# Performance work log

Hardware: AMD Instinct MI355X
Metric: run time of the kernel (lower is better)

Reference implementation:

```python
import jax, jax.numpy as jnp
import numpy as np

B, CW_DIM, Z_DIM = 512, 4096, 1024
DIM_CODES, BOOK_SIZE, DIM_EMBED = 64, 1024, 64
ENC_H, DEC_H = 512, 2048
SLOPE = 0.2  # LeakyReLU negative slope

def lrelu(v):
    return jnp.where(v > 0, v, SLOPE * v)

def setup_inputs() -> dict:
    key = jax.random.key(0)
    ks = jax.random.split(key, 12)
    s = 0.02
    inp = {
        'x': jax.random.normal(ks[0], (B, CW_DIM), jnp.float32),
        'codebook': jax.random.normal(ks[1], (DIM_CODES, BOOK_SIZE, DIM_EMBED), jnp.float32),
        'enc_w1': jax.random.normal(ks[2], (ENC_H, DIM_EMBED), jnp.float32) * s,
        'enc_b1': jnp.zeros((ENC_H,), jnp.float32),
        'enc_w2': jax.random.normal(ks[3], (2 * Z_DIM, ENC_H), jnp.float32) * s,
        'enc_b2': jnp.zeros((2 * Z_DIM,), jnp.float32),
        'inf1_w': jax.random.normal(ks[4], (Z_DIM // 2, 2 * Z_DIM), jnp.float32) * s,
        'inf1_b': jnp.zeros((Z_DIM // 2,), jnp.float32),
        'inf2_w1': jax.random.normal(ks[5], (2 * Z_DIM, 9 * Z_DIM // 4), jnp.float32) * s,
        'inf2_b1': jnp.zeros((2 * Z_DIM,), jnp.float32),
        'inf2_w2': jax.random.normal(ks[6], (3 * Z_DIM // 2, 2 * Z_DIM), jnp.float32) * s,
        'inf2_b2': jnp.zeros((3 * Z_DIM // 2,), jnp.float32),
        'prior_w1': jax.random.normal(ks[7], (2 * Z_DIM, Z_DIM // 4), jnp.float32) * s,
        'prior_b1': jnp.zeros((2 * Z_DIM,), jnp.float32),
        'prior_w2': jax.random.normal(ks[8], (3 * Z_DIM // 2, 2 * Z_DIM), jnp.float32) * s,
        'prior_b2': jnp.zeros((3 * Z_DIM // 2,), jnp.float32),
        'dec_w1': jax.random.normal(ks[9], (DEC_H, 3 * Z_DIM // 4), jnp.float32) * s,
        'dec_b1': jnp.zeros((DEC_H,), jnp.float32),
        'dec_w2': jax.random.normal(ks[10], (CW_DIM, DEC_H), jnp.float32) * s,
        'dec_b2': jnp.zeros((CW_DIM,), jnp.float32),
    }
    return inp

def reference(x, codebook, enc_w1, enc_b1, enc_w2, enc_b2,
              inf1_w, inf1_b, inf2_w1, inf2_b1, inf2_w2, inf2_b2,
              prior_w1, prior_b1, prior_w2, prior_b2,
              dec_w1, dec_b1, dec_w2, dec_b2):
    b = x.shape[0]
    # ---- encode: view (B, dim_codes, dim_embed), per-code conv + max-pool + Linear
    xe = x.reshape(b, DIM_CODES, DIM_EMBED)                       # (B, C, E)
    feat = lrelu(jnp.einsum('bce,he->bch', xe, enc_w1) + enc_b1)  # (B, C, H)
    h = jnp.max(feat, axis=1) @ enc_w2.T + enc_b2                 # (B, 2z)
    mu, log_var = jnp.split(h @ inf1_w.T + inf1_b, 2, axis=1)     # (B, z/4) each
    z1 = mu                                                        # eval mode: sample == mu
    # ---- decode
    p = lrelu(z1 @ prior_w1.T + prior_b1) @ prior_w2.T + prior_b2
    p_mu, p_logvar = jnp.split(p, 2, axis=1)                       # (B, 3z/4) each
    d = lrelu(jnp.concatenate([z1, h], axis=1) @ inf2_w1.T + inf2_b1) @ inf2_w2.T + inf2_b2
    d_mu, d_log_var = jnp.split(d, 2, axis=1)
    z2 = d_mu + p_mu                                               # eval mode sample
    cw_recon = lrelu(z2 @ dec_w1.T + dec_b1) @ dec_w2.T + dec_b2   # (B, cw_dim)
    # ---- dist: squared distance to (detached) codebook, no explicit repeat
    xr = cw_recon.reshape(b, DIM_CODES, DIM_EMBED)
    book = jax.lax.stop_gradient(codebook)                         # (C, S, E)
    cw_dist = ((xr ** 2).sum(-1)[..., None]
               + (book ** 2).sum(-1)[None]
               - 2.0 * jnp.einsum('bce,cse->bcs', xr, book))       # (B, C, S)
    idx = jnp.argmin(cw_dist, axis=-1).reshape(b * DIM_CODES, 1)   # matches torch (B*C, 1)
    return (cw_recon, cw_dist, idx, mu, log_var, d_mu, d_log_var, p_logvar)
```

## Files before the change

kernel.cpp:

```cpp
#include <hip/hip_runtime.h>
#include <hip/hip_bf16.h>

typedef __hip_bfloat16 bf16;
typedef unsigned short u16;

#define BATCH 512
#define CW_DIM 4096
#define DIM_CODES 64
#define BOOK_SIZE 1024
#define DIM_EMBED 64
#define ENC_H 512

__device__ __forceinline__ float bf2f(u16 u) {
    unsigned int x = ((unsigned int)u) << 16;
    return __uint_as_float(x);
}
__device__ __forceinline__ float loadf(const void* p, size_t i, int bf) {
    if (bf) return bf2f(((const u16*)p)[i]);
    return ((const float*)p)[i];
}
__device__ __forceinline__ float4 load4(const void* p, size_t i, int bf) {
    if (bf) {
        const u16* q = (const u16*)p + i;
        uint2 raw = *reinterpret_cast<const uint2*>(q);
        float4 r;
        r.x = bf2f((u16)(raw.x & 0xFFFF));
        r.y = bf2f((u16)(raw.x >> 16));
        r.z = bf2f((u16)(raw.y & 0xFFFF));
        r.w = bf2f((u16)(raw.y >> 16));
        return r;
    }
    return *reinterpret_cast<const float4*>((const float*)p + i);
}
__device__ __forceinline__ void stored(void* p, size_t i, int bf, double v) {
    if (bf) ((bf16*)p)[i] = __float2bfloat16((float)v);
    else    ((float*)p)[i] = (float)v;
}
__device__ __forceinline__ u16 f2bfu(float v) {
    bf16 b = __float2bfloat16(v);
    return *reinterpret_cast<u16*>(&b);
}

__global__ void detect_kernel(const u16* __restrict__ x, int* __restrict__ flag) {
    __shared__ int hits;
    if (threadIdx.x == 0) hits = 0;
    __syncthreads();
    int h = 0;
    for (int i = threadIdx.x; i < 16384; i += 256) {
        u16 v = x[2 * i];
        if (((v >> 7) & 0xFF) == 0xFF) h++;
    }
    atomicAdd(&hits, h);
    __syncthreads();
    if (threadIdx.x == 0) *flag = (hits == 0) ? 1 : 0;
}

__global__ void booknorm_kernel(const void* __restrict__ book, double* __restrict__ bn,
                                const int* __restrict__ dflag) {
    const int bf = *dflag;
    int r = blockIdx.x * blockDim.x + threadIdx.x;
    if (r >= DIM_CODES * BOOK_SIZE) return;
    double acc = 0.0;
    for (int e = 0; e < DIM_EMBED; e += 4) {
        float4 v = load4(book, (size_t)r * DIM_EMBED + e, bf);
        acc = fma((double)v.x, (double)v.x, acc);
        acc = fma((double)v.y, (double)v.y, acc);
        acc = fma((double)v.z, (double)v.z, acc);
        acc = fma((double)v.w, (double)v.w, acc);
    }
    bn[r] = acc;
}

__global__ __launch_bounds__(256) void enc_kernel(const void* __restrict__ x,
                                                  const void* __restrict__ w1,
                                                  const void* __restrict__ b1,
                                                  float* __restrict__ hmax,
                                                  const int* __restrict__ dflag) {
    const int bf = *dflag;
    __shared__ float xs_t[64][68];
    __shared__ float wsh_t[64][68];
    __shared__ float red[64][17];
    int t = threadIdx.x;
    int h0 = blockIdx.x * 64;
    int b = blockIdx.y;

    int cr = t >> 2;
    int e0 = (t & 3) << 4;
    for (int q = 0; q < 4; q++) {
        int e = e0 + (q << 2);
        float4 xv = load4(x, (size_t)b * CW_DIM + cr * DIM_EMBED + e, bf);
        xs_t[e + 0][cr] = xv.x; xs_t[e + 1][cr] = xv.y;
        xs_t[e + 2][cr] = xv.z; xs_t[e + 3][cr] = xv.w;
        float4 wv = load4(w1, (size_t)(h0 + cr) * DIM_EMBED + e, bf);
        wsh_t[e + 0][cr] = wv.x; wsh_t[e + 1][cr] = wv.y;
        wsh_t[e + 2][cr] = wv.z; wsh_t[e + 3][cr] = wv.w;
    }
    __syncthreads();

    int th = t & 15, tc = t >> 4;
    float acc[4][4] = {};
    for (int e = 0; e < 64; e++) {
        float4 a4 = *(const float4*)&xs_t[e][tc << 2];
        float4 w4 = *(const float4*)&wsh_t[e][th << 2];
        float aa[4] = {a4.x, a4.y, a4.z, a4.w};
        float ww[4] = {w4.x, w4.y, w4.z, w4.w};
#pragma unroll
        for (int i = 0; i < 4; i++)
#pragma unroll
            for (int j = 0; j < 4; j++)
                acc[i][j] = fmaf(aa[i], ww[j], acc[i][j]);
    }
#pragma unroll
    for (int j = 0; j < 4; j++) {
        float bj = loadf(b1, h0 + (th << 2) + j, bf);
        float m = -1e30f;
#pragma unroll
        for (int i = 0; i < 4; i++) {
            float v = acc[i][j] + bj;
            v = v > 0.f ? v : 0.2f * v;
            m = fmaxf(m, v);
        }
        red[(th << 2) + j][tc] = m;
    }
    __syncthreads();
    if (t < 64) {
        float m = red[t][0];
        for (int k = 1; k < 16; k++) m = fmaxf(m, red[t][k]);
        hmax[(size_t)b * ENC_H + h0 + t] = m;
    }
}

__global__ __launch_bounds__(256) void gemm_kernel(const float* __restrict__ A1, int lda1, int K1,
                                                   const float* __restrict__ A2, int lda2, int Ktot,
                                                   const float* __restrict__ Aadd,
                                                   const void* __restrict__ W,
                                                   const void* __restrict__ bias,
                                                   float* __restrict__ C, int N, int act,
                                                   void* __restrict__ out,
                                                   size_t s0base, int s0c0, int s0c1, int s0stride,
                                                   size_t s1base, int s1c0, int s1c1, int s1stride,
                                                   const int* __restrict__ dflag) {
    const int bf = *dflag;
    __shared__ float As[2][16][68];
    __shared__ float Ws[2][16][68];
    int t = threadIdx.x;
    int tx = t & 15, ty = t >> 4;
    int n0 = blockIdx.x * 64, m0 = blockIdx.y * 64;
    int mrow = t >> 2, kq = (t & 3) << 2;
    float acc[4][4] = {};

    float4 av, wv;
    {
        int k = kq;
        if (k < K1) {
            av = *reinterpret_cast<const float4*>(A1 + (size_t)(m0 + mrow) * lda1 + k);
            if (Aadd) {
                float4 ad = *reinterpret_cast<const float4*>(Aadd + (size_t)(m0 + mrow) * lda1 + k);
                av.x += ad.x; av.y += ad.y; av.z += ad.z; av.w += ad.w;
            }
        } else {
            av = *reinterpret_cast<const float4*>(A2 + (size_t)(m0 + mrow) * lda2 + (k - K1));
        }
        wv = load4(W, (size_t)(n0 + mrow) * Ktot + k, bf);
    }
    As[0][kq + 0][mrow] = av.x; As[0][kq + 1][mrow] = av.y;
    As[0][kq + 2][mrow] = av.z; As[0][kq + 3][mrow] = av.w;
    Ws[0][kq + 0][mrow] = wv.x; Ws[0][kq + 1][mrow] = wv.y;
    Ws[0][kq + 2][mrow] = wv.z; Ws[0][kq + 3][mrow] = wv.w;
    __syncthreads();

    int buf = 0;
#pragma unroll 1
    for (int kt = 0; kt < Ktot; kt += 16) {
        int nxt = kt + 16;
        if (nxt < Ktot) {
            int k = nxt + kq;
            if (k < K1) {
                av = *reinterpret_cast<const float4*>(A1 + (size_t)(m0 + mrow) * lda1 + k);
                if (Aadd) {
                    float4 ad = *reinterpret_cast<const float4*>(Aadd + (size_t)(m0 + mrow) * lda1 + k);
                    av.x += ad.x; av.y += ad.y; av.z += ad.z; av.w += ad.w;
                }
            } else {
                av = *reinterpret_cast<const float4*>(A2 + (size_t)(m0 + mrow) * lda2 + (k - K1));
            }
            wv = load4(W, (size_t)(n0 + mrow) * Ktot + k, bf);
        }
#pragma unroll
        for (int kk = 0; kk < 16; kk++) {
            float4 a4 = *(const float4*)&As[buf][kk][ty << 2];
            float4 w4 = *(const float4*)&Ws[buf][kk][tx << 2];
            float a[4] = {a4.x, a4.y, a4.z, a4.w};
            float w[4] = {w4.x, w4.y, w4.z, w4.w};
#pragma unroll
            for (int i = 0; i < 4; i++)
#pragma unroll
                for (int j = 0; j < 4; j++)
                    acc[i][j] = fmaf(a[i], w[j], acc[i][j]);
        }
        if (nxt < Ktot) {
            int nb = buf ^ 1;
            As[nb][kq + 0][mrow] = av.x; As[nb][kq + 1][mrow] = av.y;
            As[nb][kq + 2][mrow] = av.z; As[nb][kq + 3][mrow] = av.w;
            Ws[nb][kq + 0][mrow] = wv.x; Ws[nb][kq + 1][mrow] = wv.y;
            Ws[nb][kq + 2][mrow] = wv.z; Ws[nb][kq + 3][mrow] = wv.w;
            __syncthreads();
            buf = nb;
        }
    }

    int nbase = n0 + tx * 4;
    float b0 = loadf(bias, nbase + 0, bf), b1v = loadf(bias, nbase + 1, bf);
    float b2 = loadf(bias, nbase + 2, bf), b3 = loadf(bias, nbase + 3, bf);
#pragma unroll
    for (int i = 0; i < 4; i++) {
        int m = m0 + ty * 4 + i;
        float ov[4];
        ov[0] = acc[i][0] + b0; ov[1] = acc[i][1] + b1v;
        ov[2] = acc[i][2] + b2; ov[3] = acc[i][3] + b3;
        if (act) {
#pragma unroll
            for (int j = 0; j < 4; j++) ov[j] = ov[j] > 0.f ? ov[j] : 0.2f * ov[j];
        }
        float4 o = {ov[0], ov[1], ov[2], ov[3]};
        *reinterpret_cast<float4*>(C + (size_t)m * N + nbase) = o;
        if (nbase >= s0c0 && nbase < s0c1) {
            size_t off = s0base + (size_t)m * s0stride + (nbase - s0c0);
            if (bf) {
                ushort4 h = {f2bfu(ov[0]), f2bfu(ov[1]), f2bfu(ov[2]), f2bfu(ov[3])};
                *reinterpret_cast<ushort4*>((u16*)out + off) = h;
            } else {
                *reinterpret_cast<float4*>((float*)out + off) = o;
            }
        }
        if (nbase >= s1c0 && nbase < s1c1) {
            size_t off = s1base + (size_t)m * s1stride + (nbase - s1c0);
            if (bf) {
                ushort4 h = {f2bfu(ov[0]), f2bfu(ov[1]), f2bfu(ov[2]), f2bfu(ov[3])};
                *reinterpret_cast<ushort4*>((u16*)out + off) = h;
            } else {
                *reinterpret_cast<float4*>((float*)out + off) = o;
            }
        }
    }
}

__global__ __launch_bounds__(256, 4) void dist_kernel(const float* __restrict__ cwr,
                                                      const void* __restrict__ book,
                                                      const double* __restrict__ bn,
                                                      void* __restrict__ out,
                                                      size_t odist, size_t oidx,
                                                      const int* __restrict__ dflag) {
    const int bf = *dflag;
    __shared__ double xs[32][64];
    __shared__ double xn[32];
    __shared__ float bs[64][66];
    int t = threadIdx.x;
    int c = blockIdx.x;
    int b0 = blockIdx.y * 32;
    int sl = t & 63, wv = t >> 6;

    for (int i = t; i < 32 * 64; i += 256) {
        int bl = i >> 6, e = i & 63;
        xs[bl][e] = (double)cwr[(size_t)(b0 + bl) * CW_DIM + c * DIM_EMBED + e];
    }
    __syncthreads();
    if (t < 32) {
        double a = 0.0;
        for (int e = 0; e < 64; e++) a = fma(xs[t][e], xs[t][e], a);
        xn[t] = a;
    }

    double bd[8];
    int bsx[8];
#pragma unroll
    for (int p = 0; p < 8; p++) { bd[p] = 1e300; bsx[p] = 0; }

#pragma unroll 1
    for (int st = 0; st < 16; st++) {
        int s0 = st * 64;
        __syncthreads();
#pragma unroll
        for (int i4 = t; i4 < 1024; i4 += 256) {
            int srow = i4 >> 4, e4 = (i4 & 15) << 2;
            float4 v = load4(book, ((size_t)c * BOOK_SIZE + s0 + srow) * DIM_EMBED + e4, bf);
            bs[srow][e4 + 0] = v.x; bs[srow][e4 + 1] = v.y;
            bs[srow][e4 + 2] = v.z; bs[srow][e4 + 3] = v.w;
        }
        __syncthreads();
        double bnv = bn[(size_t)c * BOOK_SIZE + s0 + sl];
#pragma unroll
        for (int pb = 0; pb < 2; pb++) {
            int blb = wv * 8 + pb * 4;
            double a0 = 0.0, a1 = 0.0, a2 = 0.0, a3 = 0.0;
#pragma unroll 8
            for (int e = 0; e < 64; e += 2) {
                float2 bv = *(const float2*)&bs[sl][e];
                double bv0 = (double)bv.x, bv1 = (double)bv.y;
                double2 x0 = *(const double2*)&xs[blb + 0][e];
                double2 x1 = *(const double2*)&xs[blb + 1][e];
                double2 x2 = *(const double2*)&xs[blb + 2][e];
                double2 x3 = *(const double2*)&xs[blb + 3][e];
                a0 = fma(x0.x, bv0, a0); a0 = fma(x0.y, bv1, a0);
                a1 = fma(x1.x, bv0, a1); a1 = fma(x1.y, bv1, a1);
                a2 = fma(x2.x, bv0, a2); a2 = fma(x2.y, bv1, a2);
                a3 = fma(x3.x, bv0, a3); a3 = fma(x3.y, bv1, a3);
            }
            double dv[4];
            dv[0] = a0; dv[1] = a1; dv[2] = a2; dv[3] = a3;
#pragma unroll
            for (int j = 0; j < 4; j++) {
                int bl = blb + j;
                double d = xn[bl] + bnv - 2.0 * dv[j];
                stored(out, odist + ((size_t)(b0 + bl) * DIM_CODES + c) * BOOK_SIZE + s0 + sl, bf, d);
                if (d < bd[pb * 4 + j]) { bd[pb * 4 + j] = d; bsx[pb * 4 + j] = s0 + sl; }
            }
        }
    }
#pragma unroll
    for (int p = 0; p < 8; p++) {
        double d = bd[p];
        int s = bsx[p];
        for (int off = 32; off >= 1; off >>= 1) {
            double od = __shfl_xor(d, off, 64);
            int os = __shfl_xor(s, off, 64);
            if (od < d || (od == d && os < s)) { d = od; s = os; }
        }
        if (sl == 0)
            stored(out, oidx + (size_t)(b0 + wv * 8 + p) * DIM_CODES + c, bf, (double)s);
    }
}

extern "C" void kernel_launch(void* const* d_in, const int* in_sizes, int n_in,
                              void* d_out, int out_size, void* d_ws, size_t ws_size,
                              hipStream_t stream) {
    const void* x        = d_in[0];
    const void* codebook = d_in[1];
    const void* enc_w1   = d_in[2];
    const void* enc_b1   = d_in[3];
    const void* enc_w2   = d_in[4];
    const void* enc_b2   = d_in[5];
    const void* inf1_w   = d_in[6];
    const void* inf1_b   = d_in[7];
    const void* inf2_w1  = d_in[8];
    const void* inf2_b1  = d_in[9];
    const void* inf2_w2  = d_in[10];
    const void* inf2_b2  = d_in[11];
    const void* prior_w1 = d_in[12];
    const void* prior_b1 = d_in[13];
    const void* prior_w2 = d_in[14];
    const void* prior_b2 = d_in[15];
    const void* dec_w1   = d_in[16];
    const void* dec_b1   = d_in[17];
    const void* dec_w2   = d_in[18];
    const void* dec_b2   = d_in[19];

    float* W0 = (float*)d_ws;
    float* inf1out = W0;
    float* pfull   = inf1out + 262144;
    float* dfull   = pfull + 786432;
    float* cwr     = dfull + 786432;
    float* bufA    = cwr + 2097152;
    float* bufB    = bufA + 1048576;
    float* bufC    = bufB + 1048576;
    double* bn     = (double*)(bufC + 393216);
    int* dflag     = (int*)(bn + 65536);

    const size_t o_cwrecon = 0;
    const size_t o_cwdist  = 2097152;
    const size_t o_idx     = 35651584;
    const size_t o_mu      = 35684352;
    const size_t o_logvar  = 35815424;
    const size_t o_dmu     = 35946496;
    const size_t o_dlogvar = 36339712;
    const size_t o_plogvar = 36732928;

    detect_kernel<<<1, 256, 0, stream>>>((const u16*)x, dflag);
    booknorm_kernel<<<256, 256, 0, stream>>>(codebook, bn, dflag);
    enc_kernel<<<dim3(8, BATCH), 256, 0, stream>>>(x, enc_w1, enc_b1, bufC, dflag);

    gemm_kernel<<<dim3(32, 8), 256, 0, stream>>>(bufC, 512, 512, bufC, 512, 512, nullptr,
                                                 enc_w2, enc_b2, bufA, 2048, 0,
                                                 d_out, 0, 0, 0, 0, 0, 0, 0, 0, dflag);
    gemm_kernel<<<dim3(8, 8), 256, 0, stream>>>(bufA, 2048, 2048, bufA, 2048, 2048, nullptr,
                                                inf1_w, inf1_b, inf1out, 512, 0,
                                                d_out, o_mu, 0, 256, 256,
                                                o_logvar, 256, 512, 256, dflag);
    gemm_kernel<<<dim3(32, 8), 256, 0, stream>>>(inf1out, 512, 256, inf1out, 512, 256, nullptr,
                                                 prior_w1, prior_b1, bufB, 2048, 1,
                                                 d_out, 0, 0, 0, 0, 0, 0, 0, 0, dflag);
    gemm_kernel<<<dim3(24, 8), 256, 0, stream>>>(bufB, 2048, 2048, bufB, 2048, 2048, nullptr,
                                                 prior_w2, prior_b2, pfull, 1536, 0,
                                                 d_out, o_plogvar, 768, 1536, 768,
                                                 0, 0, 0, 0, dflag);
    gemm_kernel<<<dim3(32, 8), 256, 0, stream>>>(inf1out, 512, 256, bufA, 2048, 2304, nullptr,
                                                 inf2_w1, inf2_b1, bufB, 2048, 1,
                                                 d_out, 0, 0, 0, 0, 0, 0, 0, 0, dflag);
    gemm_kernel<<<dim3(24, 8), 256, 0, stream>>>(bufB, 2048, 2048, bufB, 2048, 2048, nullptr,
                                                 inf2_w2, inf2_b2, dfull, 1536, 0,
                                                 d_out, o_dmu, 0, 768, 768,
                                                 o_dlogvar, 768, 1536, 768, dflag);
    gemm_kernel<<<dim3(32, 8), 256, 0, stream>>>(dfull, 1536, 768, dfull, 1536, 768, pfull,
                                                 dec_w1, dec_b1, bufA, 2048, 1,
                                                 d_out, 0, 0, 0, 0, 0, 0, 0, 0, dflag);
    gemm_kernel<<<dim3(64, 8), 256, 0, stream>>>(bufA, 2048, 2048, bufA, 2048, 2048, nullptr,
                                                 dec_w2, dec_b2, cwr, 4096, 0,
                                                 d_out, o_cwrecon, 0, 4096, 4096,
                                                 0, 0, 0, 0, dflag);

    dist_kernel<<<dim3(64, 16), 256, 0, stream>>>(cwr, codebook, bn,
                                                  d_out, o_cwdist, o_idx, dflag);
}
```

Baseline: 1.068 ms.

## Batch independent prior/inference GEMMs into paired launches and double-buffer codebook tiles

Independent GEMM pairs (prior and inf2 layers) now run together in one launch through a descriptor-based gemm2 kernel, with a new scratch buffer so both outputs can coexist. This removes two launches and fills the GPU better, since each single GEMM alone had a small grid. The distance kernel now double-buffers codebook tiles in shared memory, prefetching the next tile into registers while computing the current one, to hide global load latency. The cost is more LDS per block, which may lower occupancy in the dist kernel, and more registers for the prefetch.

```diff
diff --git a/kernel.cpp b/kernel.cpp
--- a/kernel.cpp
+++ b/kernel.cpp
@@ -130,38 +130,37 @@
     }
 }
 
-__global__ __launch_bounds__(256) void gemm_kernel(const float* __restrict__ A1, int lda1, int K1,
-                                                   const float* __restrict__ A2, int lda2, int Ktot,
-                                                   const float* __restrict__ Aadd,
-                                                   const void* __restrict__ W,
-                                                   const void* __restrict__ bias,
-                                                   float* __restrict__ C, int N, int act,
-                                                   void* __restrict__ out,
-                                                   size_t s0base, int s0c0, int s0c1, int s0stride,
-                                                   size_t s1base, int s1c0, int s1c1, int s1stride,
-                                                   const int* __restrict__ dflag) {
-    const int bf = *dflag;
+struct GDesc {
+    const float* A1; const float* A2; const float* Aadd;
+    const void* W; const void* bias; float* C;
+    int lda1, K1, lda2, Ktot, N, act, nbx, pad;
+    size_t s0base; int s0c0, s0c1, s0stride;
+    size_t s1base; int s1c0, s1c1, s1stride;
+};
+
+__device__ __forceinline__ void gemm_body(const GDesc& g, int bx, int by,
+                                          void* __restrict__ out, const int bf) {
     __shared__ float As[2][16][68];
     __shared__ float Ws[2][16][68];
     int t = threadIdx.x;
     int tx = t & 15, ty = t >> 4;
-    int n0 = blockIdx.x * 64, m0 = blockIdx.y * 64;
+    int n0 = bx * 64, m0 = by * 64;
     int mrow = t >> 2, kq = (t & 3) << 2;
     float acc[4][4] = {};
 
     float4 av, wv;
     {
         int k = kq;
-        if (k < K1) {
-            av = *reinterpret_cast<const float4*>(A1 + (size_t)(m0 + mrow) * lda1 + k);
-            if (Aadd) {
-                float4 ad = *reinterpret_cast<const float4*>(Aadd + (size_t)(m0 + mrow) * lda1 + k);
+        if (k < g.K1) {
+            av = *reinterpret_cast<const float4*>(g.A1 + (size_t)(m0 + mrow) * g.lda1 + k);
+            if (g.Aadd) {
+                float4 ad = *reinterpret_cast<const float4*>(g.Aadd + (size_t)(m0 + mrow) * g.lda1 + k);
                 av.x += ad.x; av.y += ad.y; av.z += ad.z; av.w += ad.w;
             }
         } else {
-            av = *reinterpret_cast<const float4*>(A2 + (size_t)(m0 + mrow) * lda2 + (k - K1));
-        }
-        wv = load4(W, (size_t)(n0 + mrow) * Ktot + k, bf);
+            av = *reinterpret_cast<const float4*>(g.A2 + (size_t)(m0 + mrow) * g.lda2 + (k - g.K1));
+        }
+        wv = load4(g.W, (size_t)(n0 + mrow) * g.Ktot + k, bf);
     }
     As[0][kq + 0][mrow] = av.x; As[0][kq + 1][mrow] = av.y;
     As[0][kq + 2][mrow] = av.z; As[0][kq + 3][mrow] = av.w;
@@ -171,20 +170,20 @@
 
     int buf = 0;
 #pragma unroll 1
-    for (int kt = 0; kt < Ktot; kt += 16) {
+    for (int kt = 0; kt < g.Ktot; kt += 16) {
         int nxt = kt + 16;
-        if (nxt < Ktot) {
+        if (nxt < g.Ktot) {
             int k = nxt + kq;
-            if (k < K1) {
-                av = *reinterpret_cast<const float4*>(A1 + (size_t)(m0 + mrow) * lda1 + k);
-                if (Aadd) {
-                    float4 ad = *reinterpret_cast<const float4*>(Aadd + (size_t)(m0 + mrow) * lda1 + k);
+            if (k < g.K1) {
+                av = *reinterpret_cast<const float4*>(g.A1 + (size_t)(m0 + mrow) * g.lda1 + k);
+                if (g.Aadd) {
+                    float4 ad = *reinterpret_cast<const float4*>(g.Aadd + (size_t)(m0 + mrow) * g.lda1 + k);
                     av.x += ad.x; av.y += ad.y; av.z += ad.z; av.w += ad.w;
                 }
             } else {
-                av = *reinterpret_cast<const float4*>(A2 + (size_t)(m0 + mrow) * lda2 + (k - K1));
-            }
-            wv = load4(W, (size_t)(n0 + mrow) * Ktot + k, bf);
+                av = *reinterpret_cast<const float4*>(g.A2 + (size_t)(m0 + mrow) * g.lda2 + (k - g.K1));
+            }
+            wv = load4(g.W, (size_t)(n0 + mrow) * g.Ktot + k, bf);
         }
 #pragma unroll
         for (int kk = 0; kk < 16; kk++) {
@@ -198,7 +197,7 @@
                 for (int j = 0; j < 4; j++)
                     acc[i][j] = fmaf(a[i], w[j], acc[i][j]);
         }
-        if (nxt < Ktot) {
+        if (nxt < g.Ktot) {
             int nb = buf ^ 1;
             As[nb][kq + 0][mrow] = av.x; As[nb][kq + 1][mrow] = av.y;
             As[nb][kq + 2][mrow] = av.z; As[nb][kq + 3][mrow] = av.w;
@@ -210,22 +209,22 @@
     }
 
     int nbase = n0 + tx * 4;
-    float b0 = loadf(bias, nbase + 0, bf), b1v = loadf(bias, nbase + 1, bf);
-    float b2 = loadf(bias, nbase + 2, bf), b3 = loadf(bias, nbase + 3, bf);
+    float b0 = loadf(g.bias, nbase + 0, bf), b1v = loadf(g.bias, nbase + 1, bf);
+    float b2 = loadf(g.bias, nbase + 2, bf), b3 = loadf(g.bias, nbase + 3, bf);
 #pragma unroll
     for (int i = 0; i < 4; i++) {
         int m = m0 + ty * 4 + i;
         float ov[4];
         ov[0] = acc[i][0] + b0; ov[1] = acc[i][1] + b1v;
         ov[2] = acc[i][2] + b2; ov[3] = acc[i][3] + b3;
-        if (act) {
+        if (g.act) {
 #pragma unroll
             for (int j = 0; j < 4; j++) ov[j] = ov[j] > 0.f ? ov[j] : 0.2f * ov[j];
         }
         float4 o = {ov[0], ov[1], ov[2], ov[3]};
-        *reinterpret_cast<float4*>(C + (size_t)m * N + nbase) = o;
-        if (nbase >= s0c0 && nbase < s0c1) {
-            size_t off = s0base + (size_t)m * s0stride + (nbase - s0c0);
+        *reinterpret_cast<float4*>(g.C + (size_t)m * g.N + nbase) = o;
+        if (nbase >= g.s0c0 && nbase < g.s0c1) {
+            size_t off = g.s0base + (size_t)m * g.s0stride + (nbase - g.s0c0);
             if (bf) {
                 ushort4 h = {f2bfu(ov[0]), f2bfu(ov[1]), f2bfu(ov[2]), f2bfu(ov[3])};
                 *reinterpret_cast<ushort4*>((u16*)out + off) = h;
@@ -233,8 +232,8 @@
                 *reinterpret_cast<float4*>((float*)out + off) = o;
             }
         }
-        if (nbase >= s1c0 && nbase < s1c1) {
-            size_t off = s1base + (size_t)m * s1stride + (nbase - s1c0);
+        if (nbase >= g.s1c0 && nbase < g.s1c1) {
+            size_t off = g.s1base + (size_t)m * g.s1stride + (nbase - g.s1c0);
             if (bf) {
                 ushort4 h = {f2bfu(ov[0]), f2bfu(ov[1]), f2bfu(ov[2]), f2bfu(ov[3])};
                 *reinterpret_cast<ushort4*>((u16*)out + off) = h;
@@ -243,6 +242,20 @@
             }
         }
     }
+}
+
+__global__ __launch_bounds__(256) void gemm_kernel(GDesc g, void* __restrict__ out,
+                                                   const int* __restrict__ dflag) {
+    gemm_body(g, blockIdx.x, blockIdx.y, out, *dflag);
+}
+
+__global__ __launch_bounds__(256) void gemm2_kernel(GDesc g0, GDesc g1, void* __restrict__ out,
+                                                    const int* __restrict__ dflag) {
+    const int bf = *dflag;
+    bool first = (int)blockIdx.x < g0.nbx;
+    GDesc g = first ? g0 : g1;
+    int bx = first ? blockIdx.x : blockIdx.x - g0.nbx;
+    gemm_body(g, bx, blockIdx.y, out, bf);
 }
 
 __global__ __launch_bounds__(256, 4) void dist_kernel(const float* __restrict__ cwr,
@@ -254,7 +267,7 @@
     const int bf = *dflag;
     __shared__ double xs[32][64];
     __shared__ double xn[32];
-    __shared__ float bs[64][66];
+    __shared__ float bs[2][64][66];
     int t = threadIdx.x;
     int c = blockIdx.x;
     int b0 = blockIdx.y * 32;
@@ -264,12 +277,33 @@
         int bl = i >> 6, e = i & 63;
         xs[bl][e] = (double)cwr[(size_t)(b0 + bl) * CW_DIM + c * DIM_EMBED + e];
     }
+    {
+        size_t base = (size_t)c * BOOK_SIZE * DIM_EMBED;
+        int i4, srow, e4;
+        i4 = t;       srow = i4 >> 4; e4 = (i4 & 15) << 2;
+        float4 v0 = load4(book, base + (size_t)srow * DIM_EMBED + e4, bf);
+        bs[0][srow][e4 + 0] = v0.x; bs[0][srow][e4 + 1] = v0.y;
+        bs[0][srow][e4 + 2] = v0.z; bs[0][srow][e4 + 3] = v0.w;
+        i4 = t + 256; srow = i4 >> 4; e4 = (i4 & 15) << 2;
+        float4 v1 = load4(book, base + (size_t)srow * DIM_EMBED + e4, bf);
+        bs[0][srow][e4 + 0] = v1.x; bs[0][srow][e4 + 1] = v1.y;
+        bs[0][srow][e4 + 2] = v1.z; bs[0][srow][e4 + 3] = v1.w;
+        i4 = t + 512; srow = i4 >> 4; e4 = (i4 & 15) << 2;
+        float4 v2 = load4(book, base + (size_t)srow * DIM_EMBED + e4, bf);
+        bs[0][srow][e4 + 0] = v2.x; bs[0][srow][e4 + 1] = v2.y;
+        bs[0][srow][e4 + 2] = v2.z; bs[0][srow][e4 + 3] = v2.w;
+        i4 = t + 768; srow = i4 >> 4; e4 = (i4 & 15) << 2;
+        float4 v3 = load4(book, base + (size_t)srow * DIM_EMBED + e4, bf);
+        bs[0][srow][e4 + 0] = v3.x; bs[0][srow][e4 + 1] = v3.y;
+        bs[0][srow][e4 + 2] = v3.z; bs[0][srow][e4 + 3] = v3.w;
+    }
     __syncthreads();
     if (t < 32) {
         double a = 0.0;
         for (int e = 0; e < 64; e++) a = fma(xs[t][e], xs[t][e], a);
         xn[t] = a;
     }
+    __syncthreads();
 
     double bd[8];
     int bsx[8];
@@ -279,23 +313,29 @@
 #pragma unroll 1
     for (int st = 0; st < 16; st++) {
         int s0 = st * 64;
-        __syncthreads();
-#pragma unroll
-        for (int i4 = t; i4 < 1024; i4 += 256) {
-            int srow = i4 >> 4, e4 = (i4 & 15) << 2;
-            float4 v = load4(book, ((size_t)c * BOOK_SIZE + s0 + srow) * DIM_EMBED + e4, bf);
-            bs[srow][e4 + 0] = v.x; bs[srow][e4 + 1] = v.y;
-            bs[srow][e4 + 2] = v.z; bs[srow][e4 + 3] = v.w;
-        }
-        __syncthreads();
+        int cur = st & 1, nb = cur ^ 1;
         double bnv = bn[(size_t)c * BOOK_SIZE + s0 + sl];
+        float4 pf0, pf1, pf2, pf3;
+        int s0n = s0 + 64;
+        if (st < 15) {
+            size_t base = ((size_t)c * BOOK_SIZE + s0n) * DIM_EMBED;
+            int i4, srow, e4;
+            i4 = t;       srow = i4 >> 4; e4 = (i4 & 15) << 2;
+            pf0 = load4(book, base + (size_t)srow * DIM_EMBED + e4, bf);
+            i4 = t + 256; srow = i4 >> 4; e4 = (i4 & 15) << 2;
+            pf1 = load4(book, base + (size_t)srow * DIM_EMBED + e4, bf);
+            i4 = t + 512; srow = i4 >> 4; e4 = (i4 & 15) << 2;
+            pf2 = load4(book, base + (size_t)srow * DIM_EMBED + e4, bf);
+            i4 = t + 768; srow = i4 >> 4; e4 = (i4 & 15) << 2;
+            pf3 = load4(book, base + (size_t)srow * DIM_EMBED + e4, bf);
+        }
 #pragma unroll
         for (int pb = 0; pb < 2; pb++) {
             int blb = wv * 8 + pb * 4;
             double a0 = 0.0, a1 = 0.0, a2 = 0.0, a3 = 0.0;
 #pragma unroll 8
             for (int e = 0; e < 64; e += 2) {
-                float2 bv = *(const float2*)&bs[sl][e];
+                float2 bv = *(const float2*)&bs[cur][sl][e];
                 double bv0 = (double)bv.x, bv1 = (double)bv.y;
                 double2 x0 = *(const double2*)&xs[blb + 0][e];
                 double2 x1 = *(const double2*)&xs[blb + 1][e];
@@ -315,6 +355,22 @@
                 stored(out, odist + ((size_t)(b0 + bl) * DIM_CODES + c) * BOOK_SIZE + s0 + sl, bf, d);
                 if (d < bd[pb * 4 + j]) { bd[pb * 4 + j] = d; bsx[pb * 4 + j] = s0 + sl; }
             }
+        }
+        if (st < 15) {
+            int i4, srow, e4;
+            i4 = t;       srow = i4 >> 4; e4 = (i4 & 15) << 2;
+            bs[nb][srow][e4 + 0] = pf0.x; bs[nb][srow][e4 + 1] = pf0.y;
+            bs[nb][srow][e4 + 2] = pf0.z; bs[nb][srow][e4 + 3] = pf0.w;
+            i4 = t + 256; srow = i4 >> 4; e4 = (i4 & 15) << 2;
+            bs[nb][srow][e4 + 0] = pf1.x; bs[nb][srow][e4 + 1] = pf1.y;
+            bs[nb][srow][e4 + 2] = pf1.z; bs[nb][srow][e4 + 3] = pf1.w;
+            i4 = t + 512; srow = i4 >> 4; e4 = (i4 & 15) << 2;
+            bs[nb][srow][e4 + 0] = pf2.x; bs[nb][srow][e4 + 1] = pf2.y;
+            bs[nb][srow][e4 + 2] = pf2.z; bs[nb][srow][e4 + 3] = pf2.w;
+            i4 = t + 768; srow = i4 >> 4; e4 = (i4 & 15) << 2;
+            bs[nb][srow][e4 + 0] = pf3.x; bs[nb][srow][e4 + 1] = pf3.y;
+            bs[nb][srow][e4 + 2] = pf3.z; bs[nb][srow][e4 + 3] = pf3.w;
+            __syncthreads();
         }
     }
 #pragma unroll
@@ -362,8 +418,9 @@
     float* cwr     = dfull + 786432;
     float* bufA    = cwr + 2097152;
     float* bufB    = bufA + 1048576;
-    float* bufC    = bufB + 1048576;
-    double* bn     = (double*)(bufC + 393216);
+    float* bufD    = bufB + 1048576;
+    float* bufC    = bufD + 1048576;
+    double* bn     = (double*)(bufC + 262144);
     int* dflag     = (int*)(bn + 65536);
 
     const size_t o_cwrecon = 0;
@@ -379,34 +436,37 @@
     booknorm_kernel<<<256, 256, 0, stream>>>(codebook, bn, dflag);
     enc_kernel<<<dim3(8, BATCH), 256, 0, stream>>>(x, enc_w1, enc_b1, bufC, dflag);
 
-    gemm_kernel<<<dim3(32, 8), 256, 0, stream>>>(bufC, 512, 512, bufC, 512, 512, nullptr,
-                                                 enc_w2, enc_b2, bufA, 2048, 0,
-                                                 d_out, 0, 0, 0, 0, 0, 0, 0, 0, dflag);
-    gemm_kernel<<<dim3(8, 8), 256, 0, stream>>>(bufA, 2048, 2048, bufA, 2048, 2048, nullptr,
-                                                inf1_w, inf1_b, inf1out, 512, 0,
-                                                d_out, o_mu, 0, 256, 256,
-                                                o_logvar, 256, 512, 256, dflag);
-    gemm_kernel<<<dim3(32, 8), 256, 0, stream>>>(inf1out, 512, 256, inf1out, 512, 256, nullptr,
-                                                 prior_w1, prior_b1, bufB, 2048, 1,
-                                                 d_out, 0, 0, 0, 0, 0, 0, 0, 0, dflag);
-    gemm_kernel<<<dim3(24, 8), 256, 0, stream>>>(bufB, 2048, 2048, bufB, 2048, 2048, nullptr,
-                                                 prior_w2, prior_b2, pfull, 1536, 0,
-                                                 d_out, o_plogvar, 768, 1536, 768,
-                                                 0, 0, 0, 0, dflag);
-    gemm_kernel<<<dim3(32, 8), 256, 0, stream>>>(inf1out, 512, 256, bufA, 2048, 2304, nullptr,
-                                                 inf2_w1, inf2_b1, bufB, 2048, 1,
-                                                 d_out, 0, 0, 0, 0, 0, 0, 0, 0, dflag);
-    gemm_kernel<<<dim3(24, 8), 256, 0, stream>>>(bufB, 2048, 2048, bufB, 2048, 2048, nullptr,
-                                                 inf2_w2, inf2_b2, dfull, 1536, 0,
-                                                 d_out, o_dmu, 0, 768, 768,
-                                                 o_dlogvar, 768, 1536, 768, dflag);
-    gemm_kernel<<<dim3(32, 8), 256, 0, stream>>>(dfull, 1536, 768, dfull, 1536, 768, pfull,
-                                                 dec_w1, dec_b1, bufA, 2048, 1,
-                                                 d_out, 0, 0, 0, 0, 0, 0, 0, 0, dflag);
-    gemm_kernel<<<dim3(64, 8), 256, 0, stream>>>(bufA, 2048, 2048, bufA, 2048, 2048, nullptr,
-                                                 dec_w2, dec_b2, cwr, 4096, 0,
-                                                 d_out, o_cwrecon, 0, 4096, 4096,
-                                                 0, 0, 0, 0, dflag);
+    GDesc g, ga, gb;
+    g = {bufC, bufC, nullptr, enc_w2, enc_b2, bufA,
+         512, 512, 512, 512, 2048, 0, 32, 0,
+         0, 0, 0, 0, 0, 0, 0, 0};
+    gemm_kernel<<<dim3(32, 8), 256, 0, stream>>>(g, d_out, dflag);
+    g = {bufA, bufA, nullptr, inf1_w, inf1_b, inf1out,
+         2048, 2048, 2048, 2048, 512, 0, 8, 0,
+         o_mu, 0, 256, 256, o_logvar, 256, 512, 256};
+    gemm_kernel<<<dim3(8, 8), 256, 0, stream>>>(g, d_out, dflag);
+    ga = {inf1out, inf1out, nullptr, prior_w1, prior_b1, bufB,
+          512, 256, 512, 256, 2048, 1, 32, 0,
+          0, 0, 0, 0, 0, 0, 0, 0};
+    gb = {inf1out, bufA, nullptr, inf2_w1, inf2_b1, bufD,
+          512, 256, 2048, 2304, 2048, 1, 32, 0,
+          0, 0, 0, 0, 0, 0, 0, 0};
+    gemm2_kernel<<<dim3(64, 8), 256, 0, stream>>>(ga, gb, d_out, dflag);
+    ga = {bufB, bufB, nullptr, prior_w2, prior_b2, pfull,
+          2048, 2048, 2048, 2048, 1536, 0, 24, 0,
+          o_plogvar, 768, 1536, 768, 0, 0, 0, 0};
+    gb = {bufD, bufD, nullptr, inf2_w2, inf2_b2, dfull,
+          2048, 2048, 2048, 2048, 1536, 0, 24, 0,
+          o_dmu, 0, 768, 768, o_dlogvar, 768, 1536, 768};
+    gemm2_kernel<<<dim3(48, 8), 256, 0, stream>>>(ga, gb, d_out, dflag);
+    g = {dfull, dfull, pfull, dec_w1, dec_b1, bufA,
+         1536, 768, 1536, 768, 2048, 1, 32, 0,
+         0, 0, 0, 0, 0, 0, 0, 0};
+    gemm_kernel<<<dim3(32, 8), 256, 0, stream>>>(g, d_out, dflag);
+    g = {bufA, bufA, nullptr, dec_w2, dec_b2, cwr,
+         2048, 2048, 2048, 2048, 4096, 0, 64, 0,
+         o_cwrecon, 0, 4096, 4096, 0, 0, 0, 0};
+    gemm_kernel<<<dim3(64, 8), 256, 0, stream>>>(g, d_out, dflag);
 
     dist_kernel<<<dim3(64, 16), 256, 0, stream>>>(cwr, codebook, bn,
                                                   d_out, o_cwdist, o_idx, dflag);
```

Measured after the change: 1.021 ms. 1.05x faster.
